# Kernel optimization log

Measured on AMD Instinct MI355X. Metric: run time of the kernel, lower is better.

The kernel has to match this reference:

```python
import jax, jax.numpy as jnp
import numpy as np

N_NODES = 50000
N_EDGES = 800000
D = 128


def gcn_conv(x, edge_index, W, b, num_nodes):
    # PyG GCNConv: h = D^{-1/2} (A + I) D^{-1/2} (x @ W) + b
    xw = x @ W  # [N, D]
    src, dst = edge_index[0], edge_index[1]
    loop = jnp.arange(num_nodes, dtype=src.dtype)
    src = jnp.concatenate([src, loop])
    dst = jnp.concatenate([dst, loop])
    deg = jax.ops.segment_sum(jnp.ones_like(dst, dtype=xw.dtype), dst,
                              num_segments=num_nodes)  # [N]
    dinv = jnp.where(deg > 0, jax.lax.rsqrt(deg), 0.0)
    norm = dinv[src] * dinv[dst]  # [E+N]
    msg = xw[src] * norm[:, None]  # gather + scale, [E+N, D]
    agg = jax.ops.segment_sum(msg, dst, num_segments=num_nodes)  # scatter-add
    return agg + b


def setup_inputs() -> dict:
    key = jax.random.key(0)
    ks = jax.random.split(key, 8)
    s = 1.0 / np.sqrt(D)
    return {
        "x": jax.random.normal(ks[0], (N_NODES, D), dtype=jnp.float32),
        "edge_index": jax.random.randint(ks[1], (2, N_EDGES), 0, N_NODES, dtype=jnp.int32),
        "Wg": jax.random.normal(ks[2], (D, D), dtype=jnp.float32) * s,
        "bg": jnp.zeros((D,), dtype=jnp.float32),
        "W1": jax.random.normal(ks[3], (D, 128), dtype=jnp.float32) * s,
        "b1": jnp.zeros((128,), dtype=jnp.float32),
        "W2": jax.random.normal(ks[4], (128, 64), dtype=jnp.float32) * (1.0 / np.sqrt(128)),
        "b2": jnp.zeros((64,), dtype=jnp.float32),
        "W3": jax.random.normal(ks[5], (64, 2), dtype=jnp.float32) * (1.0 / np.sqrt(64)),
        "b3": jnp.zeros((2,), dtype=jnp.float32),
    }


def reference(x, edge_index, Wg, bg, W1, b1, W2, b2, W3, b3):
    out = jax.nn.relu(gcn_conv(x, edge_index, Wg, bg, x.shape[0]))
    h = out + x  # residual
    h = jax.nn.relu(h @ W1 + b1)
    h = jax.nn.relu(h @ W2 + b2)
    h = h @ W3 + b3  # [N, 2]
    return (h[:, 0], h[:, 1])
```

## Files before the change

kernel.cpp:

```cpp
#include <hip/hip_runtime.h>

#define TD 256
#define BCAP 3072

typedef unsigned int uint;
typedef unsigned short ushort;
typedef __attribute__((ext_vector_type(8))) short bf16x8;
typedef __attribute__((ext_vector_type(4))) float f32x4;

__device__ __forceinline__ ushort f2bf(float f) {
    uint u = __float_as_uint(f);
    u += 0x7fffu + ((u >> 16) & 1u);
    return (ushort)(u >> 16);
}
__device__ __forceinline__ float2 bfp2f(uint u) {
    float2 r;
    r.x = __uint_as_float(u << 16);
    r.y = __uint_as_float(u & 0xffff0000u);
    return r;
}

__global__ void k_prep(const float* __restrict__ Wg, const float* __restrict__ W1,
                       const float* __restrict__ W2,
                       ushort* __restrict__ Wgf, ushort* __restrict__ W1f,
                       ushort* __restrict__ W2f,
                       int* __restrict__ bucketCursor, int nbuck) {
    int tid0 = blockIdx.x * TD + threadIdx.x;
    int stride = gridDim.x * TD;
    for (int i = tid0; i < nbuck; i += stride) bucketCursor[i] = 0;
    for (int id = tid0; id < 2048; id += stride) {
        int lane = id & 63;
        int col = ((id >> 8) << 4) + (lane & 15);
        int k0 = ((id >> 6) & 3) * 32 + (lane >> 4) * 8;
        #pragma unroll
        for (int j = 0; j < 8; j++) {
            Wgf[id * 8 + j] = f2bf(Wg[(k0 + j) * 128 + col]);
            W1f[id * 8 + j] = f2bf(W1[(k0 + j) * 128 + col]);
        }
    }
    for (int id = tid0; id < 1024; id += stride) {
        int lane = id & 63;
        int col = ((id >> 8) << 4) + (lane & 15);
        int k0 = ((id >> 6) & 3) * 32 + (lane >> 4) * 8;
        #pragma unroll
        for (int j = 0; j < 8; j++)
            W2f[id * 8 + j] = f2bf(W2[(k0 + j) * 64 + col]);
    }
}

__global__ __launch_bounds__(256) void kb_bin(const int* __restrict__ src,
                                              const int* __restrict__ dst, int e,
                                              int nbuck,
                                              int* __restrict__ bucketCursor,
                                              uint* __restrict__ binned) {
    __shared__ int hist[512];
    __shared__ int base[512];
    __shared__ int cur[512];
    int t = threadIdx.x;
    int per = (e + gridDim.x - 1) / gridDim.x;
    int e0 = blockIdx.x * per;
    int e1 = min(e0 + per, e);
    for (int i = t; i < nbuck; i += TD) hist[i] = 0;
    __syncthreads();
    for (int i = e0 + t; i < e1; i += TD)
        atomicAdd(&hist[dst[i] >> 7], 1);
    __syncthreads();
    for (int i = t; i < nbuck; i += TD) {
        int c = hist[i];
        base[i] = (c > 0) ? atomicAdd(&bucketCursor[i], c) : 0;
        cur[i] = 0;
    }
    __syncthreads();
    for (int i = e0 + t; i < e1; i += TD) {
        int d = dst[i];
        int b = d >> 7;
        int pos = base[b] + atomicAdd(&cur[b], 1);
        if (pos < BCAP)
            binned[(size_t)b * BCAP + pos] = ((uint)src[i] << 7) | (uint)(d & 127);
    }
}

__global__ __launch_bounds__(256) void kb_fill(const int* __restrict__ bucketCursor,
                                               const uint* __restrict__ binned,
                                               int n, int nbuck,
                                               int* __restrict__ deg,
                                               int* __restrict__ rowStart,
                                               float* __restrict__ dinv,
                                               int* __restrict__ csr) {
    __shared__ int d128[128];
    __shared__ int sc[128];
    __shared__ int rs128[128];
    __shared__ int cur128[128];
    __shared__ int wsum[4];
    int b = blockIdx.x;
    int t = threadIdx.x;

    int part = 0;
    for (int i = t; i < b; i += TD) part += bucketCursor[i];
    #pragma unroll
    for (int m = 1; m < 64; m <<= 1) part += __shfl_xor(part, m);
    if ((t & 63) == 0) wsum[t >> 6] = part;
    if (t < 128) { d128[t] = 0; cur128[t] = 0; }
    __syncthreads();
    int base = wsum[0] + wsum[1] + wsum[2] + wsum[3];
    int cnt = min(bucketCursor[b], BCAP);
    int node0 = b << 7;

    for (int i = t; i < cnt; i += TD)
        atomicAdd(&d128[binned[(size_t)b * BCAP + i] & 127], 1);
    __syncthreads();
    int v = (t < 128) ? d128[t] : 0;
    if (t < 128) sc[t] = v;
    __syncthreads();
    for (int off = 1; off < 128; off <<= 1) {
        int u = (t < 128 && t >= off) ? sc[t - off] : 0;
        __syncthreads();
        if (t < 128) sc[t] += u;
        __syncthreads();
    }
    if (t < 128) {
        int node = node0 + t;
        if (node < n) {
            int rs = base + sc[t] - v;
            rs128[t] = rs;
            rowStart[node] = rs;
            deg[node] = v;
            dinv[node] = rsqrtf((float)(v + 1));
        }
    }
    __syncthreads();
    for (int i = t; i < cnt; i += TD) {
        uint pk = binned[(size_t)b * BCAP + i];
        int loc = pk & 127;
        int slot = rs128[loc] + atomicAdd(&cur128[loc], 1);
        csr[slot] = (int)(pk >> 7);
    }
}

__global__ __launch_bounds__(256) void k_xw(const float* __restrict__ x,
                                            const ushort* __restrict__ Wgf,
                                            const float* __restrict__ dinv,
                                            ushort* __restrict__ xws,
                                            int n, int nt16) {
    __shared__ ushort sW[16384];
    int t = threadIdx.x;
    for (int i = t; i < 2048; i += TD)
        ((float4*)sW)[i] = ((const float4*)Wgf)[i];
    __syncthreads();

    int wave = t >> 6, lane = t & 63;
    int quad = lane >> 4, m = lane & 15;

    for (int tile = blockIdx.x * 4 + wave; tile < nt16; tile += gridDim.x * 4) {
        int row0 = tile * 16;
        int arow = min(row0 + m, n - 1);
        const float* pa = x + (size_t)arow * 128 + quad * 8;
        bf16x8 af[4];
        #pragma unroll
        for (int kc = 0; kc < 4; kc++) {
            float4 f0 = *(const float4*)(pa + kc * 32);
            float4 f1 = *(const float4*)(pa + kc * 32 + 4);
            union { bf16x8 v; ushort u[8]; } tmp;
            tmp.u[0] = f2bf(f0.x); tmp.u[1] = f2bf(f0.y);
            tmp.u[2] = f2bf(f0.z); tmp.u[3] = f2bf(f0.w);
            tmp.u[4] = f2bf(f1.x); tmp.u[5] = f2bf(f1.y);
            tmp.u[6] = f2bf(f1.z); tmp.u[7] = f2bf(f1.w);
            af[kc] = tmp.v;
        }
        int orow[4]; float dv[4];
        #pragma unroll
        for (int i = 0; i < 4; i++) {
            orow[i] = row0 + quad * 4 + i;
            dv[i] = (orow[i] < n) ? dinv[orow[i]] : 0.f;
        }
        #pragma unroll
        for (int c16 = 0; c16 < 8; c16++) {
            f32x4 acc = {0.f, 0.f, 0.f, 0.f};
            #pragma unroll
            for (int kc = 0; kc < 4; kc++) {
                bf16x8 bf = *(const bf16x8*)&sW[((c16 * 4 + kc) * 64 + lane) * 8];
                acc = __builtin_amdgcn_mfma_f32_16x16x32_bf16(af[kc], bf, acc, 0, 0, 0);
            }
            int col = c16 * 16 + m;
            #pragma unroll
            for (int i = 0; i < 4; i++)
                if (orow[i] < n)
                    xws[(size_t)orow[i] * 128 + col] = f2bf(acc[i] * dv[i]);
        }
    }
}

__global__ __launch_bounds__(256) void k_agg(const uint* __restrict__ xws,
                                             const float* __restrict__ x,
                                             const int* __restrict__ rowStart,
                                             const int* __restrict__ deg,
                                             const int* __restrict__ csr,
                                             const float* __restrict__ dinv,
                                             const float* __restrict__ bg,
                                             ushort* __restrict__ h0b, int n) {
    int wave = threadIdx.x >> 6;
    int lane = threadIdx.x & 63;
    int node = blockIdx.x * 4 + wave;
    if (node >= n) return;
    float2 A0, A1 = {0.f,0.f}, A2 = {0.f,0.f}, A3 = {0.f,0.f};
    A0 = bfp2f(xws[(size_t)node * 64 + lane]);
    int st = rowStart[node];
    int cnt = deg[node];
    int i = 0;
    for (; i + 8 <= cnt; i += 8) {
        int s0 = csr[st + i + 0], s1 = csr[st + i + 1];
        int s2 = csr[st + i + 2], s3 = csr[st + i + 3];
        int s4 = csr[st + i + 4], s5 = csr[st + i + 5];
        int s6 = csr[st + i + 6], s7 = csr[st + i + 7];
        uint u0 = xws[(size_t)s0 * 64 + lane];
        uint u1 = xws[(size_t)s1 * 64 + lane];
        uint u2 = xws[(size_t)s2 * 64 + lane];
        uint u3 = xws[(size_t)s3 * 64 + lane];
        uint u4 = xws[(size_t)s4 * 64 + lane];
        uint u5 = xws[(size_t)s5 * 64 + lane];
        uint u6 = xws[(size_t)s6 * 64 + lane];
        uint u7 = xws[(size_t)s7 * 64 + lane];
        float2 v0 = bfp2f(u0), v1 = bfp2f(u1), v2 = bfp2f(u2), v3 = bfp2f(u3);
        float2 v4 = bfp2f(u4), v5 = bfp2f(u5), v6 = bfp2f(u6), v7 = bfp2f(u7);
        A0.x += v0.x; A0.y += v0.y;  A1.x += v1.x; A1.y += v1.y;
        A2.x += v2.x; A2.y += v2.y;  A3.x += v3.x; A3.y += v3.y;
        A0.x += v4.x; A0.y += v4.y;  A1.x += v5.x; A1.y += v5.y;
        A2.x += v6.x; A2.y += v6.y;  A3.x += v7.x; A3.y += v7.y;
    }
    for (; i < cnt; i++) {
        int s = csr[st + i];
        float2 v = bfp2f(xws[(size_t)s * 64 + lane]);
        A0.x += v.x; A0.y += v.y;
    }
    float2 acc;
    acc.x = (A0.x + A1.x) + (A2.x + A3.x);
    acc.y = (A0.y + A1.y) + (A2.y + A3.y);
    float dv = dinv[node];
    float2 b = ((const float2*)bg)[lane];
    float2 xv = ((const float2*)x)[(size_t)node * 64 + lane];
    float ox = fmaxf(acc.x * dv + b.x, 0.f) + xv.x;
    float oy = fmaxf(acc.y * dv + b.y, 0.f) + xv.y;
    uint up = ((uint)f2bf(oy) << 16) | (uint)f2bf(ox);
    ((uint*)h0b)[(size_t)node * 64 + lane] = up;
}

__global__ __launch_bounds__(256) void k_fc1(const ushort* __restrict__ h0b,
                                             const ushort* __restrict__ W1f,
                                             const float* __restrict__ b1,
                                             ushort* __restrict__ h1b,
                                             int n, int nt16) {
    __shared__ ushort sW[16384];
    int t = threadIdx.x;
    for (int i = t; i < 2048; i += TD)
        ((float4*)sW)[i] = ((const float4*)W1f)[i];
    __syncthreads();

    int wave = t >> 6, lane = t & 63;
    int quad = lane >> 4, m = lane & 15;
    float bc[8];
    #pragma unroll
    for (int c16 = 0; c16 < 8; c16++) bc[c16] = b1[c16 * 16 + m];

    for (int tile = blockIdx.x * 4 + wave; tile < nt16; tile += gridDim.x * 4) {
        int row0 = tile * 16;
        int arow = min(row0 + m, n - 1);
        const ushort* pa = h0b + (size_t)arow * 128 + quad * 8;
        bf16x8 af[4];
        #pragma unroll
        for (int kc = 0; kc < 4; kc++)
            af[kc] = *(const bf16x8*)(pa + kc * 32);
        #pragma unroll
        for (int c16 = 0; c16 < 8; c16++) {
            f32x4 acc = {0.f, 0.f, 0.f, 0.f};
            #pragma unroll
            for (int kc = 0; kc < 4; kc++) {
                bf16x8 bf = *(const bf16x8*)&sW[((c16 * 4 + kc) * 64 + lane) * 8];
                acc = __builtin_amdgcn_mfma_f32_16x16x32_bf16(af[kc], bf, acc, 0, 0, 0);
            }
            int col = c16 * 16 + m;
            #pragma unroll
            for (int i = 0; i < 4; i++) {
                int r = row0 + quad * 4 + i;
                if (r < n)
                    h1b[(size_t)r * 128 + col] = f2bf(fmaxf(acc[i] + bc[c16], 0.f));
            }
        }
    }
}

__global__ __launch_bounds__(256) void k_fc23(const ushort* __restrict__ h1b,
                                              const ushort* __restrict__ W2f,
                                              const float* __restrict__ b2,
                                              const float* __restrict__ W3,
                                              const float* __restrict__ b3,
                                              float* __restrict__ out,
                                              int n, int nt16) {
    __shared__ ushort sW[8192];
    int t = threadIdx.x;
    for (int i = t; i < 1024; i += TD)
        ((float4*)sW)[i] = ((const float4*)W2f)[i];
    __syncthreads();

    int wave = t >> 6, lane = t & 63;
    int quad = lane >> 4, m = lane & 15;
    float bc[4], w30[4], w31[4];
    #pragma unroll
    for (int c16 = 0; c16 < 4; c16++) {
        int col = c16 * 16 + m;
        bc[c16]  = b2[col];
        w30[c16] = W3[col * 2 + 0];
        w31[c16] = W3[col * 2 + 1];
    }
    float b30 = b3[0], b31 = b3[1];

    for (int tile = blockIdx.x * 4 + wave; tile < nt16; tile += gridDim.x * 4) {
        int row0 = tile * 16;
        int arow = min(row0 + m, n - 1);
        const ushort* pa = h1b + (size_t)arow * 128 + quad * 8;
        bf16x8 af[4];
        #pragma unroll
        for (int kc = 0; kc < 4; kc++)
            af[kc] = *(const bf16x8*)(pa + kc * 32);
        float p0[4] = {}, p1[4] = {};
        #pragma unroll
        for (int c16 = 0; c16 < 4; c16++) {
            f32x4 acc = {0.f, 0.f, 0.f, 0.f};
            #pragma unroll
            for (int kc = 0; kc < 4; kc++) {
                bf16x8 bf = *(const bf16x8*)&sW[((c16 * 4 + kc) * 64 + lane) * 8];
                acc = __builtin_amdgcn_mfma_f32_16x16x32_bf16(af[kc], bf, acc, 0, 0, 0);
            }
            #pragma unroll
            for (int i = 0; i < 4; i++) {
                float h2 = fmaxf(acc[i] + bc[c16], 0.f);
                p0[i] += h2 * w30[c16];
                p1[i] += h2 * w31[c16];
            }
        }
        #pragma unroll
        for (int i = 0; i < 4; i++) {
            #pragma unroll
            for (int msk = 1; msk < 16; msk <<= 1) {
                p0[i] += __shfl_xor(p0[i], msk);
                p1[i] += __shfl_xor(p1[i], msk);
            }
        }
        if (m == 0) {
            #pragma unroll
            for (int i = 0; i < 4; i++) {
                int r = row0 + quad * 4 + i;
                if (r < n) {
                    out[r] = p0[i] + b30;
                    out[(size_t)n + r] = p1[i] + b31;
                }
            }
        }
    }
}


extern "C" void kernel_launch(void* const* d_in, const int* in_sizes, int n_in,
                              void* d_out, int out_size, void* d_ws, size_t ws_size,
                              hipStream_t stream) {
    const float* x  = (const float*)d_in[0];
    const int*   ei = (const int*)d_in[1];
    const float* Wg = (const float*)d_in[2];
    const float* bg = (const float*)d_in[3];
    const float* W1 = (const float*)d_in[4];
    const float* b1 = (const float*)d_in[5];
    const float* W2 = (const float*)d_in[6];
    const float* b2 = (const float*)d_in[7];
    const float* W3 = (const float*)d_in[8];
    const float* b3 = (const float*)d_in[9];
    float* out = (float*)d_out;

    int n = in_sizes[0] / 128;
    int e = in_sizes[1] / 2;
    const int* src = ei;
    const int* dst = ei + e;

    char* ws = (char*)d_ws;
    size_t off = 0;
    auto alloc = [&](size_t bytes) -> void* {
        void* p = ws + off;
        off = (off + bytes + 255) & ~(size_t)255;
        return p;
    };
    int nbuck = (n + 127) >> 7;
    int*    deg      = (int*)alloc(sizeof(int) * (size_t)n);
    int*    rowStart = (int*)alloc(sizeof(int) * (size_t)n);
    float*  dinv     = (float*)alloc(sizeof(float) * (size_t)n);
    int*    bucketCursor = (int*)alloc(sizeof(int) * 512);
    uint*   binned   = (uint*)alloc(sizeof(uint) * (size_t)nbuck * BCAP);
    int*    csr      = (int*)alloc(sizeof(int) * (size_t)e);
    ushort* xws      = (ushort*)alloc(sizeof(ushort) * (size_t)n * 128);
    ushort* h0b      = (ushort*)alloc(sizeof(ushort) * (size_t)n * 128);
    ushort* h1b      = (ushort*)alloc(sizeof(ushort) * (size_t)n * 128);
    ushort* Wgf      = (ushort*)alloc(sizeof(ushort) * 16384);
    ushort* W1f      = (ushort*)alloc(sizeof(ushort) * 16384);
    ushort* W2f      = (ushort*)alloc(sizeof(ushort) * 8192);
    (void)ws_size; (void)n_in; (void)out_size;

    int nt16 = (n + 15) / 16;

    hipLaunchKernelGGL(k_prep,  dim3(20),  dim3(TD), 0, stream,
                       Wg, W1, W2, Wgf, W1f, W2f, bucketCursor, nbuck);
    hipLaunchKernelGGL(kb_bin,  dim3(96),  dim3(TD), 0, stream,
                       src, dst, e, nbuck, bucketCursor, binned);
    hipLaunchKernelGGL(kb_fill, dim3(nbuck), dim3(TD), 0, stream,
                       bucketCursor, binned, n, nbuck, deg, rowStart, dinv, csr);
    hipLaunchKernelGGL(k_xw,    dim3(784), dim3(TD), 0, stream, x, Wgf, dinv, xws, n, nt16);
    hipLaunchKernelGGL(k_agg,   dim3((n + 3) / 4), dim3(TD), 0, stream,
                       (const uint*)xws, x, rowStart, deg, csr, dinv, bg, h0b, n);
    hipLaunchKernelGGL(k_fc1,   dim3(784), dim3(TD), 0, stream, h0b, W1f, b1, h1b, n, nt16);
    hipLaunchKernelGGL(k_fc23,  dim3(784), dim3(TD), 0, stream, h1b, W2f, b2, W3, b3, out, n, nt16);
}
```

Baseline: 193.2 us.

## Fuse MLP layers via per-wave LDS staging and merge weight prep into binning

Fuses the fc1 and fc2/fc3 kernels into one MLP kernel. Each wave writes its 16x128 ReLU tile to a padded LDS buffer and reloads it as the A operand for the second MFMA, so the h1 intermediate never goes to global memory. W2 fragments are now read straight from global memory instead of LDS. Weight conversion is folded into the binning kernel using extra blocks, and the cursor reset becomes a memset, which cuts one launch and overlaps the prep with binning.

```diff
diff --git a/kernel.cpp b/kernel.cpp
--- a/kernel.cpp
+++ b/kernel.cpp
@@ -2,6 +2,7 @@
 
 #define TD 256
 #define BCAP 3072
+#define BINB 96
 
 typedef unsigned int uint;
 typedef unsigned short ushort;
@@ -20,63 +21,60 @@
     return r;
 }
 
-__global__ void k_prep(const float* __restrict__ Wg, const float* __restrict__ W1,
-                       const float* __restrict__ W2,
-                       ushort* __restrict__ Wgf, ushort* __restrict__ W1f,
-                       ushort* __restrict__ W2f,
-                       int* __restrict__ bucketCursor, int nbuck) {
-    int tid0 = blockIdx.x * TD + threadIdx.x;
-    int stride = gridDim.x * TD;
-    for (int i = tid0; i < nbuck; i += stride) bucketCursor[i] = 0;
-    for (int id = tid0; id < 2048; id += stride) {
-        int lane = id & 63;
-        int col = ((id >> 8) << 4) + (lane & 15);
-        int k0 = ((id >> 6) & 3) * 32 + (lane >> 4) * 8;
-        #pragma unroll
-        for (int j = 0; j < 8; j++) {
-            Wgf[id * 8 + j] = f2bf(Wg[(k0 + j) * 128 + col]);
-            W1f[id * 8 + j] = f2bf(W1[(k0 + j) * 128 + col]);
-        }
-    }
-    for (int id = tid0; id < 1024; id += stride) {
-        int lane = id & 63;
-        int col = ((id >> 8) << 4) + (lane & 15);
-        int k0 = ((id >> 6) & 3) * 32 + (lane >> 4) * 8;
-        #pragma unroll
-        for (int j = 0; j < 8; j++)
-            W2f[id * 8 + j] = f2bf(W2[(k0 + j) * 64 + col]);
-    }
-}
-
-__global__ __launch_bounds__(256) void kb_bin(const int* __restrict__ src,
-                                              const int* __restrict__ dst, int e,
-                                              int nbuck,
-                                              int* __restrict__ bucketCursor,
-                                              uint* __restrict__ binned) {
+__global__ __launch_bounds__(256) void k_prep_bin(
+        const float* __restrict__ Wg, const float* __restrict__ W1,
+        const float* __restrict__ W2,
+        ushort* __restrict__ Wgf, ushort* __restrict__ W1f, ushort* __restrict__ W2f,
+        const int* __restrict__ src, const int* __restrict__ dst, int e,
+        int nbuck, int* __restrict__ bucketCursor, uint* __restrict__ binned) {
     __shared__ int hist[512];
     __shared__ int base[512];
     __shared__ int cur[512];
     int t = threadIdx.x;
-    int per = (e + gridDim.x - 1) / gridDim.x;
-    int e0 = blockIdx.x * per;
-    int e1 = min(e0 + per, e);
-    for (int i = t; i < nbuck; i += TD) hist[i] = 0;
-    __syncthreads();
-    for (int i = e0 + t; i < e1; i += TD)
-        atomicAdd(&hist[dst[i] >> 7], 1);
-    __syncthreads();
-    for (int i = t; i < nbuck; i += TD) {
-        int c = hist[i];
-        base[i] = (c > 0) ? atomicAdd(&bucketCursor[i], c) : 0;
-        cur[i] = 0;
-    }
-    __syncthreads();
-    for (int i = e0 + t; i < e1; i += TD) {
-        int d = dst[i];
-        int b = d >> 7;
-        int pos = base[b] + atomicAdd(&cur[b], 1);
-        if (pos < BCAP)
-            binned[(size_t)b * BCAP + pos] = ((uint)src[i] << 7) | (uint)(d & 127);
+
+    if (blockIdx.x < BINB) {
+        int per = (e + BINB - 1) / BINB;
+        int e0 = blockIdx.x * per;
+        int e1 = min(e0 + per, e);
+        for (int i = t; i < nbuck; i += TD) hist[i] = 0;
+        __syncthreads();
+        for (int i = e0 + t; i < e1; i += TD)
+            atomicAdd(&hist[dst[i] >> 7], 1);
+        __syncthreads();
+        for (int i = t; i < nbuck; i += TD) {
+            int c = hist[i];
+            base[i] = (c > 0) ? atomicAdd(&bucketCursor[i], c) : 0;
+            cur[i] = 0;
+        }
+        __syncthreads();
+        for (int i = e0 + t; i < e1; i += TD) {
+            int d = dst[i];
+            int b = d >> 7;
+            int pos = base[b] + atomicAdd(&cur[b], 1);
+            if (pos < BCAP)
+                binned[(size_t)b * BCAP + pos] = ((uint)src[i] << 7) | (uint)(d & 127);
+        }
+    } else {
+        int tid0 = (blockIdx.x - BINB) * TD + t;
+        int stride = (gridDim.x - BINB) * TD;
+        for (int id = tid0; id < 2048; id += stride) {
+            int lane = id & 63;
+            int col = ((id >> 8) << 4) + (lane & 15);
+            int k0 = ((id >> 6) & 3) * 32 + (lane >> 4) * 8;
+            #pragma unroll
+            for (int j = 0; j < 8; j++) {
+                Wgf[id * 8 + j] = f2bf(Wg[(k0 + j) * 128 + col]);
+                W1f[id * 8 + j] = f2bf(W1[(k0 + j) * 128 + col]);
+            }
+        }
+        for (int id = tid0; id < 1024; id += stride) {
+            int lane = id & 63;
+            int col = ((id >> 8) << 4) + (lane & 15);
+            int k0 = ((id >> 6) & 3) * 32 + (lane >> 4) * 8;
+            #pragma unroll
+            for (int j = 0; j < 8; j++)
+                W2f[id * 8 + j] = f2bf(W2[(k0 + j) * 64 + col]);
+        }
     }
 }
 
@@ -142,7 +140,7 @@
                                             const float* __restrict__ dinv,
                                             ushort* __restrict__ xws,
                                             int n, int nt16) {
-    __shared__ ushort sW[16384];
+    __shared__ __align__(16) ushort sW[16384];
     int t = threadIdx.x;
     for (int i = t; i < 2048; i += TD)
         ((float4*)sW)[i] = ((const float4*)Wgf)[i];
@@ -244,22 +242,38 @@
     ((uint*)h0b)[(size_t)node * 64 + lane] = up;
 }
 
-__global__ __launch_bounds__(256) void k_fc1(const ushort* __restrict__ h0b,
+__global__ __launch_bounds__(256) void k_mlp(const ushort* __restrict__ h0b,
                                              const ushort* __restrict__ W1f,
+                                             const ushort* __restrict__ W2f,
                                              const float* __restrict__ b1,
-                                             ushort* __restrict__ h1b,
+                                             const float* __restrict__ b2,
+                                             const float* __restrict__ W3,
+                                             const float* __restrict__ b3,
+                                             float* __restrict__ out,
                                              int n, int nt16) {
-    __shared__ ushort sW[16384];
+    __shared__ __align__(16) ushort sW1[16384];
+    __shared__ __align__(16) ushort tb[4][16 * 136];
     int t = threadIdx.x;
     for (int i = t; i < 2048; i += TD)
-        ((float4*)sW)[i] = ((const float4*)W1f)[i];
+        ((float4*)sW1)[i] = ((const float4*)W1f)[i];
     __syncthreads();
 
     int wave = t >> 6, lane = t & 63;
     int quad = lane >> 4, m = lane & 15;
-    float bc[8];
+    ushort* tw = &tb[wave][0];
+
+    float bc1[8];
     #pragma unroll
-    for (int c16 = 0; c16 < 8; c16++) bc[c16] = b1[c16 * 16 + m];
+    for (int c = 0; c < 8; c++) bc1[c] = b1[c * 16 + m];
+    float bc2[4], w30[4], w31[4];
+    #pragma unroll
+    for (int c = 0; c < 4; c++) {
+        int col = c * 16 + m;
+        bc2[c] = b2[col];
+        w30[c] = W3[col * 2 + 0];
+        w31[c] = W3[col * 2 + 1];
+    }
+    float b30 = b3[0], b31 = b3[1];
 
     for (int tile = blockIdx.x * 4 + wave; tile < nt16; tile += gridDim.x * 4) {
         int row0 = tile * 16;
@@ -269,70 +283,38 @@
         #pragma unroll
         for (int kc = 0; kc < 4; kc++)
             af[kc] = *(const bf16x8*)(pa + kc * 32);
+
         #pragma unroll
         for (int c16 = 0; c16 < 8; c16++) {
             f32x4 acc = {0.f, 0.f, 0.f, 0.f};
             #pragma unroll
             for (int kc = 0; kc < 4; kc++) {
-                bf16x8 bf = *(const bf16x8*)&sW[((c16 * 4 + kc) * 64 + lane) * 8];
+                bf16x8 bf = *(const bf16x8*)&sW1[((c16 * 4 + kc) * 64 + lane) * 8];
                 acc = __builtin_amdgcn_mfma_f32_16x16x32_bf16(af[kc], bf, acc, 0, 0, 0);
             }
             int col = c16 * 16 + m;
             #pragma unroll
-            for (int i = 0; i < 4; i++) {
-                int r = row0 + quad * 4 + i;
-                if (r < n)
-                    h1b[(size_t)r * 128 + col] = f2bf(fmaxf(acc[i] + bc[c16], 0.f));
-            }
-        }
-    }
-}
-
-__global__ __launch_bounds__(256) void k_fc23(const ushort* __restrict__ h1b,
-                                              const ushort* __restrict__ W2f,
-                                              const float* __restrict__ b2,
-                                              const float* __restrict__ W3,
-                                              const float* __restrict__ b3,
-                                              float* __restrict__ out,
-                                              int n, int nt16) {
-    __shared__ ushort sW[8192];
-    int t = threadIdx.x;
-    for (int i = t; i < 1024; i += TD)
-        ((float4*)sW)[i] = ((const float4*)W2f)[i];
-    __syncthreads();
-
-    int wave = t >> 6, lane = t & 63;
-    int quad = lane >> 4, m = lane & 15;
-    float bc[4], w30[4], w31[4];
-    #pragma unroll
-    for (int c16 = 0; c16 < 4; c16++) {
-        int col = c16 * 16 + m;
-        bc[c16]  = b2[col];
-        w30[c16] = W3[col * 2 + 0];
-        w31[c16] = W3[col * 2 + 1];
-    }
-    float b30 = b3[0], b31 = b3[1];
-
-    for (int tile = blockIdx.x * 4 + wave; tile < nt16; tile += gridDim.x * 4) {
-        int row0 = tile * 16;
-        int arow = min(row0 + m, n - 1);
-        const ushort* pa = h1b + (size_t)arow * 128 + quad * 8;
-        bf16x8 af[4];
+            for (int i = 0; i < 4; i++)
+                tw[(quad * 4 + i) * 136 + col] = f2bf(fmaxf(acc[i] + bc1[c16], 0.f));
+        }
+
+        bf16x8 a2[4];
         #pragma unroll
         for (int kc = 0; kc < 4; kc++)
-            af[kc] = *(const bf16x8*)(pa + kc * 32);
+            a2[kc] = *(const bf16x8*)&tw[m * 136 + kc * 32 + quad * 8];
+
         float p0[4] = {}, p1[4] = {};
         #pragma unroll
         for (int c16 = 0; c16 < 4; c16++) {
             f32x4 acc = {0.f, 0.f, 0.f, 0.f};
             #pragma unroll
             for (int kc = 0; kc < 4; kc++) {
-                bf16x8 bf = *(const bf16x8*)&sW[((c16 * 4 + kc) * 64 + lane) * 8];
-                acc = __builtin_amdgcn_mfma_f32_16x16x32_bf16(af[kc], bf, acc, 0, 0, 0);
+                bf16x8 bf = *(const bf16x8*)&W2f[((c16 * 4 + kc) * 64 + lane) * 8];
+                acc = __builtin_amdgcn_mfma_f32_16x16x32_bf16(a2[kc], bf, acc, 0, 0, 0);
             }
             #pragma unroll
             for (int i = 0; i < 4; i++) {
-                float h2 = fmaxf(acc[i] + bc[c16], 0.f);
+                float h2 = fmaxf(acc[i] + bc2[c16], 0.f);
                 p0[i] += h2 * w30[c16];
                 p1[i] += h2 * w31[c16];
             }
@@ -395,7 +377,6 @@
     int*    csr      = (int*)alloc(sizeof(int) * (size_t)e);
     ushort* xws      = (ushort*)alloc(sizeof(ushort) * (size_t)n * 128);
     ushort* h0b      = (ushort*)alloc(sizeof(ushort) * (size_t)n * 128);
-    ushort* h1b      = (ushort*)alloc(sizeof(ushort) * (size_t)n * 128);
     ushort* Wgf      = (ushort*)alloc(sizeof(ushort) * 16384);
     ushort* W1f      = (ushort*)alloc(sizeof(ushort) * 16384);
     ushort* W2f      = (ushort*)alloc(sizeof(ushort) * 8192);
@@ -403,15 +384,15 @@
 
     int nt16 = (n + 15) / 16;
 
-    hipLaunchKernelGGL(k_prep,  dim3(20),  dim3(TD), 0, stream,
-                       Wg, W1, W2, Wgf, W1f, W2f, bucketCursor, nbuck);
-    hipLaunchKernelGGL(kb_bin,  dim3(96),  dim3(TD), 0, stream,
+    hipMemsetAsync(bucketCursor, 0, sizeof(int) * 512, stream);
+    hipLaunchKernelGGL(k_prep_bin, dim3(BINB + 20), dim3(TD), 0, stream,
+                       Wg, W1, W2, Wgf, W1f, W2f,
                        src, dst, e, nbuck, bucketCursor, binned);
     hipLaunchKernelGGL(kb_fill, dim3(nbuck), dim3(TD), 0, stream,
                        bucketCursor, binned, n, nbuck, deg, rowStart, dinv, csr);
     hipLaunchKernelGGL(k_xw,    dim3(784), dim3(TD), 0, stream, x, Wgf, dinv, xws, n, nt16);
     hipLaunchKernelGGL(k_agg,   dim3((n + 3) / 4), dim3(TD), 0, stream,
                        (const uint*)xws, x, rowStart, deg, csr, dinv, bg, h0b, n);
-    hipLaunchKernelGGL(k_fc1,   dim3(784), dim3(TD), 0, stream, h0b, W1f, b1, h1b, n, nt16);
-    hipLaunchKernelGGL(k_fc23,  dim3(784), dim3(TD), 0, stream, h1b, W2f, b2, W3, b3, out, n, nt16);
-}
+    hipLaunchKernelGGL(k_mlp,   dim3(784), dim3(TD), 0, stream,
+                       h0b, W1f, W2f, b1, b2, W3, b3, out, n, nt16);
+}
```

After: 188.9 us. -2.2%, faster.
